# Performance work log

Measured on AMD Instinct MI355X. Metric: run time of the kernel, lower is better.

Reference implementation:

```python
import jax, jax.numpy as jnp
import numpy as np

FSIZE = 5
PAD = FSIZE // 2


def _conv(mosaick, filts):
    # mosaick [B,1,H,W], filts [f,f,K] -> responses [B,K,H,W].
    # Cross-correlation with edge-clamped boundary (Halide clamp semantics).
    x = jnp.pad(mosaick, ((0, 0), (0, 0), (PAD, PAD), (PAD, PAD)), mode='edge')
    k = jnp.transpose(filts, (2, 0, 1))[:, None, :, :]  # [K,1,f,f] OIHW
    return jax.lax.conv_general_dilated(
        x, k, window_strides=(1, 1), padding='VALID',
        dimension_numbers=('NCHW', 'OIHW', 'NCHW'))


def setup_inputs() -> dict:
    key = jax.random.key(0)
    k1, k2, k3 = jax.random.split(key, 3)
    B, H, W, K, f = 16, 512, 512, 8, FSIZE
    std = 1.0 / (f * f)  # matches normal_(0, 1/(fsize*fsize))
    return {
        'mosaick': jax.random.normal(k1, (B, 1, H, W), dtype=jnp.float32),
        'sel_filts': jax.random.normal(k2, (f, f, K), dtype=jnp.float32) * std,
        'green_filts': jax.random.normal(k3, (f, f, K), dtype=jnp.float32) * std,
    }


def reference(mosaick, sel_filts, green_filts):
    # Per-pixel soft filter selection over K candidate green-interpolation filters.
    sel = _conv(mosaick, sel_filts)      # [B,K,H,W] selection scores
    grn = _conv(mosaick, green_filts)    # [B,K,H,W] candidate green estimates
    w = jax.nn.softmax(sel, axis=1)      # softmax over filter bank
    interp = jnp.sum(w * grn, axis=1, keepdims=True)  # [B,1,H,W]
    # GRBG Bayer: green where row parity == col parity; copy known greens.
    H, W = mosaick.shape[-2], mosaick.shape[-1]
    yy = jnp.arange(H)[:, None]
    xx = jnp.arange(W)[None, :]
    is_green = (yy % 2) == (xx % 2)      # [H,W] bool
    # Output green channel only (module returns output[:, 1:2, ...]).
    return jnp.where(is_green, mosaick, interp)
```

## Files before the change

kernel.cpp:

```cpp
#include <hip/hip_runtime.h>


typedef float f32x16 __attribute__((ext_vector_type(16)));
typedef short s16x8  __attribute__((ext_vector_type(8)));

#define HH 512
#define WW 512
#define TW 64
#define TH 32
#define RS 80
#define NROW 36
#define NEL 72

__device__ __forceinline__ unsigned short bf16rne(float x) {
    unsigned u = __float_as_uint(x);
    u += 0x7fffu + ((u >> 16) & 1u);
    return (unsigned short)(u >> 16);
}
__device__ __forceinline__ int pk2(float hi, float lo) {
    return (int)((((unsigned)bf16rne(hi)) << 16) | (unsigned)bf16rne(lo));
}
__device__ __forceinline__ float hi16(int v) { return __uint_as_float(((unsigned)v) & 0xffff0000u); }
__device__ __forceinline__ float lo16(int v) { return __uint_as_float(((unsigned)v) << 16); }
__device__ __forceinline__ float bf2f(unsigned short s) {
    return __uint_as_float(((unsigned)s) << 16);
}

__global__ void build_frags_kernel(const float* __restrict__ sf,
                                   const float* __restrict__ gf,
                                   short* __restrict__ ws)
{
    const int lane = threadIdx.x;
    const int mm   = lane & 31;
    const int h    = (lane >> 5) & 1;
    const int c    = mm >> 1;
    const bool tg  = mm & 1;
    const bool chok = mm < 16;
    const float* fb = tg ? gf : sf;

    s16x8 A[6];
#pragma unroll
    for (int f = 0; f < 6; ++f)
#pragma unroll
        for (int j = 0; j < 8; ++j) A[f][j] = 0;

#pragma unroll
    for (int j = 0; j < 8; ++j) {
        const int dx0 = j - 1;
        if (dx0 >= 0 && dx0 < 5 && chok) {
            A[0][j] = (short)bf16rne(fb[((h)     * 5 + dx0) * 8 + c]);
            A[1][j] = (short)bf16rne(fb[((2 + h) * 5 + dx0) * 8 + c]);
            if (h == 0)
                A[2][j] = (short)bf16rne(fb[(4 * 5 + dx0) * 8 + c]);
        }
        const int dx1 = j;
        if (dx1 < 5 && chok) {
            if (h == 1)
                A[3][j] = (short)bf16rne(fb[(0 * 5 + dx1) * 8 + c]);
            A[4][j] = (short)bf16rne(fb[((1 + h) * 5 + dx1) * 8 + c]);
            A[5][j] = (short)bf16rne(fb[((3 + h) * 5 + dx1) * 8 + c]);
        }
    }
    s16x8* dst = (s16x8*)(ws + lane * 48);
#pragma unroll
    for (int f = 0; f < 6; ++f) dst[f] = A[f];
}

__global__ __launch_bounds__(256) void demosaick_kernel(
    const float* __restrict__ mos,
    const short* __restrict__ frg,
    float* __restrict__ out)
{
    __shared__ alignas(16) unsigned short tileS[NROW * RS];

    const int tid   = threadIdx.x;
    const int bx    = blockIdx.x;
    const int by    = blockIdx.y;
    const int bimg  = blockIdx.z;
    const int tileX = bx * TW;
    const int tileY = by * TH;
    const float* img = mos + (size_t)bimg * HH * WW;

    const int lane = tid & 63;
    const int w    = tid >> 6;
    const int n    = lane & 31;
    const int h    = lane >> 5;

    const s16x8* wsf = (const s16x8*)(frg + lane * 48);
    const s16x8 Aa0 = wsf[0], Ab0 = wsf[1], Ac0 = wsf[2];
    const s16x8 Aa1 = wsf[3], Ab1 = wsf[4], Ac1 = wsf[5];

    const bool interior = (bx >= 1) && (bx <= 6) && (by >= 1) && (by <= 14);
    if (interior) {
        for (int i = tid; i < NROW * 9; i += 256) {
            int r = i / 9, s = i - 9 * r;
            const float2* src = (const float2*)(img + (size_t)(tileY - 2 + r) * WW
                                                + (tileX - 2 + 8 * s));
            float2 v0 = src[0], v1 = src[1], v2 = src[2], v3 = src[3];
            int4 d;
            d.x = pk2(v0.y, v0.x);
            d.y = pk2(v1.y, v1.x);
            d.z = pk2(v2.y, v2.x);
            d.w = pk2(v3.y, v3.x);
            *(int4*)&tileS[r * RS + 8 * s] = d;
        }
    } else {
        for (int i = tid; i < NROW * NEL; i += 256) {
            int r = i / NEL, e = i - NEL * r;
            int gy = min(max(tileY - 2 + r, 0), HH - 1);
            int gx = min(max(tileX - 2 + e, 0), WW - 1);
            tileS[r * RS + e] = bf16rne(img[(size_t)gy * WW + gx]);
        }
    }
    __syncthreads();

    const int* tb = (const int*)tileS;
    float* outp = out + (size_t)bimg * HH * WW;

    union U { int4 v; s16x8 s; };
    U B0, B1, B2;
    {
        const int ia0 = (8 * w + h) * 40 + n;
        B0.v.x = tb[ia0];       B0.v.y = tb[ia0 + 1];
        B0.v.z = tb[ia0 + 2];   B0.v.w = tb[ia0 + 3];
        B1.v.x = tb[ia0 + 80];  B1.v.y = tb[ia0 + 81];
        B1.v.z = tb[ia0 + 82];  B1.v.w = tb[ia0 + 83];
        B2.v.x = tb[ia0 + 160]; B2.v.y = tb[ia0 + 161];
        B2.v.z = tb[ia0 + 162]; B2.v.w = tb[ia0 + 163];
    }

#pragma unroll
    for (int pp = 0; pp < 4; ++pp) {
        const int Rl = 8 * w + 2 * pp;
        const int y  = tileY + Rl;

        f32x16 a0 = (f32x16)(0.f), a1 = (f32x16)(0.f);
        a0 = __builtin_amdgcn_mfma_f32_32x32x16_bf16(Aa0, B0.s, a0, 0, 0, 0);
        a1 = __builtin_amdgcn_mfma_f32_32x32x16_bf16(Aa1, B0.s, a1, 0, 0, 0);
        a0 = __builtin_amdgcn_mfma_f32_32x32x16_bf16(Ab0, B1.s, a0, 0, 0, 0);
        a1 = __builtin_amdgcn_mfma_f32_32x32x16_bf16(Ab1, B1.s, a1, 0, 0, 0);
        a0 = __builtin_amdgcn_mfma_f32_32x32x16_bf16(Ac0, B2.s, a0, 0, 0, 0);
        a1 = __builtin_amdgcn_mfma_f32_32x32x16_bf16(Ac1, B2.s, a1, 0, 0, 0);

        if (pp < 3) {
            B0 = B1; B1 = B2;
            const int ia = (Rl + 6 + h) * 40 + n;
            B2.v.x = tb[ia];     B2.v.y = tb[ia + 1];
            B2.v.z = tb[ia + 2]; B2.v.w = tb[ia + 3];
        }

        float den0 = 0.f, num0 = 0.f, den1 = 0.f, num1 = 0.f;
#pragma unroll
        for (int j = 0; j < 4; ++j) {
            float e0 = __expf(a0[2 * j]);
            den0 += e0;
            num0 = fmaf(e0, a0[2 * j + 1], num0);
            float e1 = __expf(a1[2 * j]);
            den1 += e1;
            num1 = fmaf(e1, a1[2 * j + 1], num1);
        }
        int ndA  = pk2(num0, den0);
        int ndB  = pk2(num1, den1);
        int ndA2 = __shfl_xor(ndA, 32);
        int ndB2 = __shfl_xor(ndB, 32);
        const float numA = num0 + hi16(ndA2);
        const float denA = den0 + lo16(ndA2);
        const float numB = num1 + hi16(ndB2);
        const float denB = den1 + lo16(ndB2);
        const float interpA = numA * __builtin_amdgcn_rcpf(denA);
        const float interpB = numB * __builtin_amdgcn_rcpf(denB);

        if (h == 0) {
            const int x0 = tileX + 2 * n;
            const float greenA = bf2f(tileS[(Rl + 2) * RS + 2 * n + 2]);
            const float greenB = bf2f(tileS[(Rl + 3) * RS + 2 * n + 3]);
            float2 stA; stA.x = greenA;  stA.y = interpA;
            float2 stB; stB.x = interpB; stB.y = greenB;
            *(float2*)(outp + (size_t)y * WW + x0)       = stA;
            *(float2*)(outp + (size_t)(y + 1) * WW + x0) = stB;
        }
    }
}

extern "C" void kernel_launch(void* const* d_in, const int* in_sizes, int n_in,
                              void* d_out, int out_size, void* d_ws, size_t ws_size,
                              hipStream_t stream) {
    const float* mos = (const float*)d_in[0];
    const float* sf  = (const float*)d_in[1];
    const float* gf  = (const float*)d_in[2];
    float* out = (float*)d_out;
    short* ws  = (short*)d_ws;

    const int B = in_sizes[0] / (HH * WW);

    build_frags_kernel<<<1, 64, 0, stream>>>(sf, gf, ws);

    dim3 grid(WW / TW, HH / TH, B);
    dim3 block(256);
    demosaick_kernel<<<grid, block, 0, stream>>>(mos, (const short*)ws, out);
}
```

Measured before the change: 86.04 us.

## Halve tile height and process two images per block with prefetch overlap

Tile height drops from 32 to 16 rows, and each block now handles image b and image b+8. The second image's global loads are issued before computing the first image, so load latency overlaps with MFMA work. B fragments are now reloaded per row pair instead of rolling through registers, and the halo overhead per output row grows with the smaller tile. The image offset of 8 is hardcoded and assumes B=16.

```diff
diff --git a/kernel.cpp b/kernel.cpp
--- a/kernel.cpp
+++ b/kernel.cpp
@@ -7,9 +7,9 @@
 #define HH 512
 #define WW 512
 #define TW 64
-#define TH 32
+#define TH 16
 #define RS 80
-#define NROW 36
+#define NROW 20
 #define NEL 72
 
 __device__ __forceinline__ unsigned short bf16rne(float x) {
@@ -66,88 +66,45 @@
     for (int f = 0; f < 6; ++f) dst[f] = A[f];
 }
 
-__global__ __launch_bounds__(256) void demosaick_kernel(
-    const float* __restrict__ mos,
-    const short* __restrict__ frg,
-    float* __restrict__ out)
-{
-    __shared__ alignas(16) unsigned short tileS[NROW * RS];
-
-    const int tid   = threadIdx.x;
-    const int bx    = blockIdx.x;
-    const int by    = blockIdx.y;
-    const int bimg  = blockIdx.z;
-    const int tileX = bx * TW;
-    const int tileY = by * TH;
-    const float* img = mos + (size_t)bimg * HH * WW;
-
-    const int lane = tid & 63;
-    const int w    = tid >> 6;
-    const int n    = lane & 31;
-    const int h    = lane >> 5;
-
-    const s16x8* wsf = (const s16x8*)(frg + lane * 48);
-    const s16x8 Aa0 = wsf[0], Ab0 = wsf[1], Ac0 = wsf[2];
-    const s16x8 Aa1 = wsf[3], Ab1 = wsf[4], Ac1 = wsf[5];
-
-    const bool interior = (bx >= 1) && (bx <= 6) && (by >= 1) && (by <= 14);
-    if (interior) {
-        for (int i = tid; i < NROW * 9; i += 256) {
-            int r = i / 9, s = i - 9 * r;
-            const float2* src = (const float2*)(img + (size_t)(tileY - 2 + r) * WW
-                                                + (tileX - 2 + 8 * s));
-            float2 v0 = src[0], v1 = src[1], v2 = src[2], v3 = src[3];
-            int4 d;
-            d.x = pk2(v0.y, v0.x);
-            d.y = pk2(v1.y, v1.x);
-            d.z = pk2(v2.y, v2.x);
-            d.w = pk2(v3.y, v3.x);
-            *(int4*)&tileS[r * RS + 8 * s] = d;
-        }
-    } else {
-        for (int i = tid; i < NROW * NEL; i += 256) {
-            int r = i / NEL, e = i - NEL * r;
-            int gy = min(max(tileY - 2 + r, 0), HH - 1);
-            int gx = min(max(tileX - 2 + e, 0), WW - 1);
-            tileS[r * RS + e] = bf16rne(img[(size_t)gy * WW + gx]);
-        }
-    }
-    __syncthreads();
-
+__device__ __forceinline__ void stage_border(
+    unsigned short* dst, const float* img, int tileX, int tileY, int tid)
+{
+    for (int i = tid; i < NROW * NEL; i += 256) {
+        int r = i / NEL, e = i - NEL * r;
+        int gy = min(max(tileY - 2 + r, 0), HH - 1);
+        int gx = min(max(tileX - 2 + e, 0), WW - 1);
+        dst[r * RS + e] = bf16rne(img[(size_t)gy * WW + gx]);
+    }
+}
+
+__device__ __forceinline__ void compute_image(
+    const unsigned short* __restrict__ tileS,
+    const s16x8& Aa0, const s16x8& Ab0, const s16x8& Ac0,
+    const s16x8& Aa1, const s16x8& Ab1, const s16x8& Ac1,
+    float* __restrict__ outp, int tileX, int tileY, int w, int n, int h)
+{
     const int* tb = (const int*)tileS;
-    float* outp = out + (size_t)bimg * HH * WW;
-
-    union U { int4 v; s16x8 s; };
-    U B0, B1, B2;
-    {
-        const int ia0 = (8 * w + h) * 40 + n;
-        B0.v.x = tb[ia0];       B0.v.y = tb[ia0 + 1];
-        B0.v.z = tb[ia0 + 2];   B0.v.w = tb[ia0 + 3];
-        B1.v.x = tb[ia0 + 80];  B1.v.y = tb[ia0 + 81];
-        B1.v.z = tb[ia0 + 82];  B1.v.w = tb[ia0 + 83];
-        B2.v.x = tb[ia0 + 160]; B2.v.y = tb[ia0 + 161];
-        B2.v.z = tb[ia0 + 162]; B2.v.w = tb[ia0 + 163];
-    }
-
-#pragma unroll
-    for (int pp = 0; pp < 4; ++pp) {
-        const int Rl = 8 * w + 2 * pp;
+#pragma unroll
+    for (int pp = 0; pp < 2; ++pp) {
+        const int Rl = 4 * w + 2 * pp;
         const int y  = tileY + Rl;
+        const int ia = (Rl + h) * 40 + n;
+
+        union { int4 v; s16x8 s; } Ba, Bb, Bc;
+        Ba.v.x = tb[ia];       Ba.v.y = tb[ia + 1];
+        Ba.v.z = tb[ia + 2];   Ba.v.w = tb[ia + 3];
+        Bb.v.x = tb[ia + 80];  Bb.v.y = tb[ia + 81];
+        Bb.v.z = tb[ia + 82];  Bb.v.w = tb[ia + 83];
+        Bc.v.x = tb[ia + 160]; Bc.v.y = tb[ia + 161];
+        Bc.v.z = tb[ia + 162]; Bc.v.w = tb[ia + 163];
 
         f32x16 a0 = (f32x16)(0.f), a1 = (f32x16)(0.f);
-        a0 = __builtin_amdgcn_mfma_f32_32x32x16_bf16(Aa0, B0.s, a0, 0, 0, 0);
-        a1 = __builtin_amdgcn_mfma_f32_32x32x16_bf16(Aa1, B0.s, a1, 0, 0, 0);
-        a0 = __builtin_amdgcn_mfma_f32_32x32x16_bf16(Ab0, B1.s, a0, 0, 0, 0);
-        a1 = __builtin_amdgcn_mfma_f32_32x32x16_bf16(Ab1, B1.s, a1, 0, 0, 0);
-        a0 = __builtin_amdgcn_mfma_f32_32x32x16_bf16(Ac0, B2.s, a0, 0, 0, 0);
-        a1 = __builtin_amdgcn_mfma_f32_32x32x16_bf16(Ac1, B2.s, a1, 0, 0, 0);
-
-        if (pp < 3) {
-            B0 = B1; B1 = B2;
-            const int ia = (Rl + 6 + h) * 40 + n;
-            B2.v.x = tb[ia];     B2.v.y = tb[ia + 1];
-            B2.v.z = tb[ia + 2]; B2.v.w = tb[ia + 3];
-        }
+        a0 = __builtin_amdgcn_mfma_f32_32x32x16_bf16(Aa0, Ba.s, a0, 0, 0, 0);
+        a1 = __builtin_amdgcn_mfma_f32_32x32x16_bf16(Aa1, Ba.s, a1, 0, 0, 0);
+        a0 = __builtin_amdgcn_mfma_f32_32x32x16_bf16(Ab0, Bb.s, a0, 0, 0, 0);
+        a1 = __builtin_amdgcn_mfma_f32_32x32x16_bf16(Ab1, Bb.s, a1, 0, 0, 0);
+        a0 = __builtin_amdgcn_mfma_f32_32x32x16_bf16(Ac0, Bc.s, a0, 0, 0, 0);
+        a1 = __builtin_amdgcn_mfma_f32_32x32x16_bf16(Ac1, Bc.s, a1, 0, 0, 0);
 
         float den0 = 0.f, num0 = 0.f, den1 = 0.f, num1 = 0.f;
 #pragma unroll
@@ -182,6 +139,82 @@
     }
 }
 
+__global__ __launch_bounds__(256) void demosaick_kernel(
+    const float* __restrict__ mos,
+    const short* __restrict__ frg,
+    float* __restrict__ out)
+{
+    __shared__ alignas(16) unsigned short tile0[NROW * RS];
+    __shared__ alignas(16) unsigned short tile1[NROW * RS];
+
+    const int tid   = threadIdx.x;
+    const int bx    = blockIdx.x;
+    const int by    = blockIdx.y;
+    const int bimg  = blockIdx.z;
+    const int tileX = bx * TW;
+    const int tileY = by * TH;
+    const float* img0 = mos + (size_t)bimg * HH * WW;
+    const float* img1 = img0 + (size_t)8 * HH * WW;
+    float* outp0 = out + (size_t)bimg * HH * WW;
+    float* outp1 = outp0 + (size_t)8 * HH * WW;
+
+    const int lane = tid & 63;
+    const int w    = tid >> 6;
+    const int n    = lane & 31;
+    const int h    = lane >> 5;
+
+    const s16x8* wsf = (const s16x8*)(frg + lane * 48);
+    const s16x8 Aa0 = wsf[0], Ab0 = wsf[1], Ac0 = wsf[2];
+    const s16x8 Aa1 = wsf[3], Ab1 = wsf[4], Ac1 = wsf[5];
+
+    const bool interior = (bx >= 1) && (bx <= 6) && (by >= 1) && (by <= 30);
+    const int r = tid / 9, s = tid - 9 * r;
+
+    if (interior) {
+        if (tid < 180) {
+            const float2* src = (const float2*)(img0 + (size_t)(tileY - 2 + r) * WW
+                                                + (tileX - 2 + 8 * s));
+            float2 v0 = src[0], v1 = src[1], v2 = src[2], v3 = src[3];
+            int4 d;
+            d.x = pk2(v0.y, v0.x);
+            d.y = pk2(v1.y, v1.x);
+            d.z = pk2(v2.y, v2.x);
+            d.w = pk2(v3.y, v3.x);
+            *(int4*)&tile0[r * RS + 8 * s] = d;
+        }
+    } else {
+        stage_border(tile0, img0, tileX, tileY, tid);
+    }
+    __syncthreads();
+
+    float2 q0, q1, q2, q3;
+    if (interior && tid < 180) {
+        const float2* src = (const float2*)(img1 + (size_t)(tileY - 2 + r) * WW
+                                            + (tileX - 2 + 8 * s));
+        q0 = src[0]; q1 = src[1]; q2 = src[2]; q3 = src[3];
+    }
+
+    compute_image(tile0, Aa0, Ab0, Ac0, Aa1, Ab1, Ac1,
+                  outp0, tileX, tileY, w, n, h);
+
+    if (interior) {
+        if (tid < 180) {
+            int4 d;
+            d.x = pk2(q0.y, q0.x);
+            d.y = pk2(q1.y, q1.x);
+            d.z = pk2(q2.y, q2.x);
+            d.w = pk2(q3.y, q3.x);
+            *(int4*)&tile1[r * RS + 8 * s] = d;
+        }
+    } else {
+        stage_border(tile1, img1, tileX, tileY, tid);
+    }
+    __syncthreads();
+
+    compute_image(tile1, Aa0, Ab0, Ac0, Aa1, Ab1, Ac1,
+                  outp1, tileX, tileY, w, n, h);
+}
+
 extern "C" void kernel_launch(void* const* d_in, const int* in_sizes, int n_in,
                               void* d_out, int out_size, void* d_ws, size_t ws_size,
                               hipStream_t stream) {
@@ -195,7 +228,7 @@
 
     build_frags_kernel<<<1, 64, 0, stream>>>(sf, gf, ws);
 
-    dim3 grid(WW / TW, HH / TH, B);
+    dim3 grid(WW / TW, HH / TH, B / 2);
     dim3 block(256);
     demosaick_kernel<<<grid, block, 0, stream>>>(mos, (const short*)ws, out);
 }
```

Result: no change. 86.25 us (+0.3%).
